# Optimization experiments

Hardware: AMD Instinct MI355X
Metric: run time of the kernel (lower is better)

The kernel has to match this reference:

```python
import jax, jax.numpy as jnp
import numpy as np

VOCAB, EMBED, HIDDEN, LAYERS = 32000, 512, 1024, 2
BATCH, SEQ = 32, 128


def gru_layer(x_tbe, h0, W_ih, W_hh, b_ih, b_hh):
    """x_tbe: [T,B,E_in]; h0: [B,H]. PyTorch GRU gate math."""
    # Precompute input-side gates for all timesteps (one big GEMM).
    gi = jnp.einsum('tbe,ge->tbg', x_tbe, W_ih) + b_ih  # [T,B,3H]

    def step(h, gi_t):
        gh = h @ W_hh.T + b_hh                      # [B,3H]
        i_r, i_z, i_n = jnp.split(gi_t, 3, axis=-1)
        h_r, h_z, h_n = jnp.split(gh, 3, axis=-1)
        r = jax.nn.sigmoid(i_r + h_r)
        z = jax.nn.sigmoid(i_z + h_z)
        n = jnp.tanh(i_n + r * h_n)
        h_new = (1.0 - z) * n + z * h
        return h_new, h_new

    hT, ys = jax.lax.scan(step, h0, gi)
    return ys, hT  # ys: [T,B,H]


def setup_inputs() -> dict:
    key = jax.random.key(0)
    ks = jax.random.split(key, 16)
    s = 0.02
    inp = {
        'inputs': jax.random.randint(ks[0], (BATCH, SEQ), 0, VOCAB),
        'lengths': jax.random.randint(ks[1], (BATCH,), 1, SEQ),
        'hidden': jax.random.normal(ks[2], (LAYERS, BATCH, HIDDEN), jnp.float32),
        'embed_table': jax.random.normal(ks[3], (VOCAB, EMBED), jnp.float32) * s,
        'W_ih_l0': jax.random.normal(ks[4], (3 * HIDDEN, EMBED), jnp.float32) * s,
        'W_hh_l0': jax.random.normal(ks[5], (3 * HIDDEN, HIDDEN), jnp.float32) * s,
        'b_ih_l0': jnp.zeros((3 * HIDDEN,), jnp.float32),
        'b_hh_l0': jnp.zeros((3 * HIDDEN,), jnp.float32),
        'W_ih_l1': jax.random.normal(ks[6], (3 * HIDDEN, HIDDEN), jnp.float32) * s,
        'W_hh_l1': jax.random.normal(ks[7], (3 * HIDDEN, HIDDEN), jnp.float32) * s,
        'b_ih_l1': jnp.zeros((3 * HIDDEN,), jnp.float32),
        'b_hh_l1': jnp.zeros((3 * HIDDEN,), jnp.float32),
        'W_out': jax.random.normal(ks[8], (VOCAB, HIDDEN), jnp.float32) * s,
        'b_out': jnp.zeros((VOCAB,), jnp.float32),
    }
    return inp


def reference(inputs, lengths, hidden, embed_table,
              W_ih_l0, W_hh_l0, b_ih_l0, b_hh_l0,
              W_ih_l1, W_hh_l1, b_ih_l1, b_hh_l1,
              W_out, b_out):
    # embedding: [B,S,E] -> time-major [S,B,E]
    x = embed_table[inputs].transpose(1, 0, 2)
    x, _ = gru_layer(x, hidden[0], W_ih_l0, W_hh_l0, b_ih_l0, b_hh_l0)
    x, _ = gru_layer(x, hidden[1], W_ih_l1, W_hh_l1, b_ih_l1, b_hh_l1)
    outputs = x.transpose(1, 0, 2)                   # [B,S,H]
    logits = outputs @ W_out.T + b_out               # [B,S,V]
    return logits
```

## Files before the change

### kernel.cpp

```cpp
#include <hip/hip_runtime.h>
#include <hip/hip_bf16.h>
#include <stdint.h>

#define T_SEQ 128
#define NBATCH 32
#define EMBED 512
#define HID 1024
#define NVOCAB 32000
#define NBLK 256

typedef float f32x4 __attribute__((ext_vector_type(4)));
typedef _Float16 f16x8 __attribute__((ext_vector_type(8)));

__device__ __forceinline__ unsigned short f2h(float f) {
  _Float16 h = (_Float16)f;
  return __builtin_bit_cast(unsigned short, h);
}
__device__ __forceinline__ float sigm(float x) {
  return 1.0f / (1.0f + __expf(-x));
}
__device__ __forceinline__ float tanh_fast(float x) {
  return 2.0f / (1.0f + __expf(-2.0f * x)) - 1.0f;
}

__global__ void k_zero(unsigned int* __restrict__ p, int n) {
  int i = blockIdx.x * blockDim.x + threadIdx.x;
  if (i < n) p[i] = 0;
}

__global__ void k_f32_to_f16(const float4* __restrict__ in,
                             ushort4* __restrict__ out, int n4) {
  int i = blockIdx.x * blockDim.x + threadIdx.x;
  int stride = gridDim.x * blockDim.x;
  for (; i < n4; i += stride) {
    float4 v = in[i];
    ushort4 o;
    o.x = f2h(v.x); o.y = f2h(v.y); o.z = f2h(v.z); o.w = f2h(v.w);
    out[i] = o;
  }
}

__global__ void k_embed(const int* __restrict__ tok, const float* __restrict__ table,
                        ushort4* __restrict__ A0) {
  int tid = blockIdx.x * 256 + threadIdx.x;
  int m = tid >> 7, kq = tid & 127;
  int b = m & 31, t = m >> 5;
  int tk = tok[b * T_SEQ + t];
  float4 v = *(const float4*)(table + (size_t)tk * EMBED + kq * 4);
  ushort4 o;
  o.x = f2h(v.x); o.y = f2h(v.y); o.z = f2h(v.z); o.w = f2h(v.w);
  A0[tid] = o;
}

#define BM 128
#define BN 128
#define BKK 64

__global__ __launch_bounds__(256) void k_gemm_bt(
    const short* __restrict__ A,
    const short* __restrict__ B,
    float* __restrict__ C,
    const float* __restrict__ bias,
    int M, int N, int K, int permute)
{
  __shared__ __align__(16) short As[BM * BKK];
  __shared__ __align__(16) short Bs[BN * BKK];
  const int tid = threadIdx.x;
  const int w = tid >> 6, l = tid & 63;
  const int wr = w >> 1, wc = w & 1;
  const int bm = blockIdx.x * BM, bn = blockIdx.y * BN;
  const int l15 = l & 15, lkg = l >> 4;

  f32x4 acc[4][4] = {};

  for (int kt = 0; kt < K; kt += BKK) {
#pragma unroll
    for (int p = 0; p < 4; ++p) {
      int idx = p * 2048 + tid * 8;
      int r = idx >> 6, c = idx & 63;
      *(f16x8*)&As[idx] = *(const f16x8*)&A[(size_t)(bm + r) * K + kt + c];
      *(f16x8*)&Bs[idx] = *(const f16x8*)&B[(size_t)(bn + r) * K + kt + c];
    }
    __syncthreads();

#pragma unroll
    for (int ks = 0; ks < 2; ++ks) {
      f16x8 af[4], bfr[4];
#pragma unroll
      for (int mi = 0; mi < 4; ++mi)
        af[mi] = *(const f16x8*)&As[(wr * 64 + mi * 16 + l15) * BKK + ks * 32 + lkg * 8];
#pragma unroll
      for (int ni = 0; ni < 4; ++ni)
        bfr[ni] = *(const f16x8*)&Bs[(wc * 64 + ni * 16 + l15) * BKK + ks * 32 + lkg * 8];
#pragma unroll
      for (int mi = 0; mi < 4; ++mi)
#pragma unroll
        for (int ni = 0; ni < 4; ++ni)
          acc[mi][ni] = __builtin_amdgcn_mfma_f32_16x16x32_f16(
              af[mi], bfr[ni], acc[mi][ni], 0, 0, 0);
    }
    __syncthreads();
  }

  const int lr = lkg * 4;
#pragma unroll
  for (int mi = 0; mi < 4; ++mi) {
#pragma unroll
    for (int ni = 0; ni < 4; ++ni) {
      int col = bn + wc * 64 + ni * 16 + l15;
      float bv = bias ? bias[col] : 0.0f;
#pragma unroll
      for (int j = 0; j < 4; ++j) {
        int row = bm + wr * 64 + mi * 16 + lr + j;
        int orow = permute ? ((row & 31) * T_SEQ + (row >> 5)) : row;
        C[(size_t)orow * N + col] = acc[mi][ni][j] + bv;
      }
    }
  }
}

__global__ __launch_bounds__(384, 2) void k_gru_fused(
    const float* __restrict__ gi0,
    const float* __restrict__ Whh0,
    const float* __restrict__ bhh0,
    const float* __restrict__ Wih1,
    const float* __restrict__ bih1,
    const float* __restrict__ Whh1,
    const float* __restrict__ bhh1,
    const _Float16* __restrict__ h0i,
    const _Float16* __restrict__ h1i,
    _Float16* __restrict__ ys0f,
    _Float16* __restrict__ ys1f,
    unsigned int* flg0,
    unsigned int* flg1,
    unsigned int* epoch0,
    unsigned int* epoch1)
{
  __shared__ float bufIH[2][3][2][64];

  const int tid = threadIdx.x;
  const int l = tid & 63;
  const int w = tid >> 6;
  const int bid = blockIdx.x;
  const int role = w >> 1, nt = w & 1;
  const int j0 = bid * 4;

  const int row16 = l & 15;
  const int jjr = row16 >> 2, gate = row16 & 3;
  const int koct = l >> 4;

  const int b_out = nt * 16 + (l & 15);
  const int j_out = j0 + (l >> 4);
  const int jj_even = (((l >> 4) & 1) == 0);

  const float* Wsrc = (role == 0) ? Whh0 : ((role == 1) ? Wih1 : Whh1);
  f16x8 af[32];
  if (gate < 3) {
    const float* wrow = Wsrc + (size_t)(gate * HID + j0 + jjr) * HID;
#pragma unroll
    for (int c = 0; c < 32; ++c) {
      float4 p0 = *(const float4*)(wrow + c * 32 + koct * 8);
      float4 p1 = *(const float4*)(wrow + c * 32 + koct * 8 + 4);
      f16x8 v = { (_Float16)p0.x, (_Float16)p0.y, (_Float16)p0.z, (_Float16)p0.w,
                  (_Float16)p1.x, (_Float16)p1.y, (_Float16)p1.z, (_Float16)p1.w };
      af[c] = v;
    }
  } else {
#pragma unroll
    for (int c = 0; c < 32; ++c) {
      f16x8 z = { (_Float16)0.f, (_Float16)0.f, (_Float16)0.f, (_Float16)0.f,
                  (_Float16)0.f, (_Float16)0.f, (_Float16)0.f, (_Float16)0.f };
      af[c] = z;
    }
  }

  float bR = 0.f, bZ = 0.f, bN = 0.f, biR = 0.f, biZ = 0.f, biN = 0.f;
  if (role == 0) {
    bR = bhh0[j_out]; bZ = bhh0[HID + j_out]; bN = bhh0[2 * HID + j_out];
  } else if (role == 2) {
    bR = bhh1[j_out]; bZ = bhh1[HID + j_out]; bN = bhh1[2 * HID + j_out];
    biR = bih1[j_out]; biZ = bih1[HID + j_out]; biN = bih1[2 * HID + j_out];
  }

  const int bfragOff = b_out * 2048 + koct * 16;

  const unsigned* ep0 = epoch0 + (bid & 7) * 64;
  const unsigned* ep1 = epoch1 + (bid & 7) * 64;

  for (int s = 0; s <= T_SEQ + 1; ++s) {
    float pre_ir = 0.f, pre_iz = 0.f, pre_in = 0.f;
    if (role == 0 && s < T_SEQ) {
      const float* gib = gi0 + (size_t)(s * NBATCH + b_out) * 3072 + j_out;
      pre_ir = gib[0]; pre_iz = gib[HID]; pre_in = gib[2 * HID];
    }

    if (bid == 0) {
      if (w == 0) {
        unsigned need0 = (s >= 1 && s <= T_SEQ) ? (unsigned)s : 0u;
        unsigned need1 = (s >= 3) ? (unsigned)(s - 2) : 0u;
        if ((need0 | need1) != 0u) {
          const unsigned* f0 = flg0 + l * 8;
          const unsigned* f1 = flg1 + l * 8;
          for (;;) {
            unsigned m0 = 0xffffffffu, m1 = 0xffffffffu;
            if (need0) {
#pragma unroll
              for (int i = 0; i < 8; ++i) {
                unsigned v = __hip_atomic_load(f0 + i, __ATOMIC_RELAXED, __HIP_MEMORY_SCOPE_AGENT);
                m0 = v < m0 ? v : m0;
              }
            }
            if (need1) {
#pragma unroll
              for (int i = 0; i < 8; ++i) {
                unsigned v = __hip_atomic_load(f1 + i, __ATOMIC_RELAXED, __HIP_MEMORY_SCOPE_AGENT);
                m1 = v < m1 ? v : m1;
              }
            }
            if (__all(m0 >= need0 && m1 >= need1)) break;
            __builtin_amdgcn_s_sleep(1);
          }
          if (l < 8) {
            if (need0)
              __hip_atomic_store(epoch0 + l * 64, need0, __ATOMIC_RELAXED, __HIP_MEMORY_SCOPE_AGENT);
            if (need1)
              __hip_atomic_store(epoch1 + l * 64, need1, __ATOMIC_RELAXED, __HIP_MEMORY_SCOPE_AGENT);
          }
          asm volatile("" ::: "memory");
        }
      }
    } else {
      unsigned need = 0;
      const unsigned* ep = ep0;
      if (role == 0) { if (s >= 1 && s < T_SEQ)  need = (unsigned)s; }
      else if (role == 1) { if (s >= 1 && s <= T_SEQ) need = (unsigned)s; }
      else { if (s >= 3) { need = (unsigned)(s - 2); ep = ep1; } }
      if (need) {
        for (;;) {
          unsigned e = __hip_atomic_load(ep, __ATOMIC_RELAXED, __HIP_MEMORY_SCOPE_AGENT);
          if (e >= need) break;
          __builtin_amdgcn_s_sleep(1);
        }
        asm volatile("" ::: "memory");
      }
    }
    __syncthreads();

    if (role == 0 && s < T_SEQ) {
      const _Float16* hsrc = (s == 0) ? h0i : (ys0f + (size_t)(s - 1) * NBATCH * HID);
      const char* hb = (const char*)hsrc + bfragOff;
      f32x4 acc0 = {}, acc1 = {};
#pragma unroll
      for (int c = 0; c < 32; c += 2) {
        f16x8 bf0 = *(const f16x8*)(hb + c * 64);
        f16x8 bf1 = *(const f16x8*)(hb + c * 64 + 64);
        acc0 = __builtin_amdgcn_mfma_f32_16x16x32_f16(af[c], bf0, acc0, 0, 0, 0);
        acc1 = __builtin_amdgcn_mfma_f32_16x16x32_f16(af[c + 1], bf1, acc1, 0, 0, 0);
      }
      f32x4 acc = acc0 + acc1;

      float hp = (float)((s == 0) ? h0i[b_out * HID + j_out]
                                  : ys0f[(size_t)((s - 1) * NBATCH + b_out) * HID + j_out]);
      float r = sigm(pre_ir + acc[0] + bR);
      float z = sigm(pre_iz + acc[1] + bZ);
      float n = tanh_fast(pre_in + r * (acc[2] + bN));
      float hnew = (1.0f - z) * n + z * hp;

      unsigned bits = (unsigned)f2h(hnew);
      unsigned hi = __shfl_down(bits, 16);
      if (jj_even) {
        unsigned packed = (bits & 0xffffu) | (hi << 16);
        __hip_atomic_store((unsigned*)(ys0f + (size_t)(s * NBATCH + b_out) * HID + j_out),
                           packed, __ATOMIC_RELAXED, __HIP_MEMORY_SCOPE_AGENT);
      }
      asm volatile("s_waitcnt vmcnt(0)" ::: "memory");
      if (l == 0)
        __hip_atomic_store(&flg0[bid * 2 + nt], (unsigned)(s + 1),
                           __ATOMIC_RELAXED, __HIP_MEMORY_SCOPE_AGENT);
    }

    if (role == 1 && s >= 1 && s <= T_SEQ) {
      const _Float16* hsrc = ys0f + (size_t)(s - 1) * NBATCH * HID;
      const char* hb = (const char*)hsrc + bfragOff;
      f32x4 acc0 = {}, acc1 = {};
#pragma unroll
      for (int c = 0; c < 32; c += 2) {
        f16x8 bf0 = *(const f16x8*)(hb + c * 64);
        f16x8 bf1 = *(const f16x8*)(hb + c * 64 + 64);
        acc0 = __builtin_amdgcn_mfma_f32_16x16x32_f16(af[c], bf0, acc0, 0, 0, 0);
        acc1 = __builtin_amdgcn_mfma_f32_16x16x32_f16(af[c + 1], bf1, acc1, 0, 0, 0);
      }
      f32x4 acc = acc0 + acc1;
      bufIH[s & 1][0][nt][l] = acc[0];
      bufIH[s & 1][1][nt][l] = acc[1];
      bufIH[s & 1][2][nt][l] = acc[2];
    }

    if (role == 2 && s >= 2) {
      const int t1 = s - 2;
      const _Float16* hsrc = (t1 == 0) ? h1i : (ys1f + (size_t)(t1 - 1) * NBATCH * HID);
      const char* hb = (const char*)hsrc + bfragOff;
      f32x4 acc0 = {}, acc1 = {};
#pragma unroll
      for (int c = 0; c < 32; c += 2) {
        f16x8 bf0 = *(const f16x8*)(hb + c * 64);
        f16x8 bf1 = *(const f16x8*)(hb + c * 64 + 64);
        acc0 = __builtin_amdgcn_mfma_f32_16x16x32_f16(af[c], bf0, acc0, 0, 0, 0);
        acc1 = __builtin_amdgcn_mfma_f32_16x16x32_f16(af[c + 1], bf1, acc1, 0, 0, 0);
      }
      f32x4 acc = acc0 + acc1;

      const int par = (s - 1) & 1;
      float ihR = bufIH[par][0][nt][l] + biR;
      float ihZ = bufIH[par][1][nt][l] + biZ;
      float ihN = bufIH[par][2][nt][l] + biN;
      float hp = (float)((t1 == 0) ? h1i[b_out * HID + j_out]
                                   : ys1f[(size_t)((t1 - 1) * NBATCH + b_out) * HID + j_out]);
      float r = sigm(ihR + acc[0] + bR);
      float z = sigm(ihZ + acc[1] + bZ);
      float n = tanh_fast(ihN + r * (acc[2] + bN));
      float hnew = (1.0f - z) * n + z * hp;

      unsigned bits = (unsigned)f2h(hnew);
      unsigned hi = __shfl_down(bits, 16);
      if (jj_even) {
        unsigned packed = (bits & 0xffffu) | (hi << 16);
        __hip_atomic_store((unsigned*)(ys1f + (size_t)(t1 * NBATCH + b_out) * HID + j_out),
                           packed, __ATOMIC_RELAXED, __HIP_MEMORY_SCOPE_AGENT);
      }
      asm volatile("s_waitcnt vmcnt(0)" ::: "memory");
      if (l == 0)
        __hip_atomic_store(&flg1[bid * 2 + nt], (unsigned)(s - 1),
                           __ATOMIC_RELAXED, __HIP_MEMORY_SCOPE_AGENT);
    }
  }
}

extern "C" void kernel_launch(void* const* d_in, const int* in_sizes, int n_in,
                              void* d_out, int out_size, void* d_ws, size_t ws_size,
                              hipStream_t stream)
{
  const int*   inputs = (const int*)d_in[0];
  const float* hidden = (const float*)d_in[2];
  const float* table  = (const float*)d_in[3];
  const float* Wih0   = (const float*)d_in[4];
  const float* Whh0   = (const float*)d_in[5];
  const float* bih0   = (const float*)d_in[6];
  const float* bhh0   = (const float*)d_in[7];
  const float* Wih1   = (const float*)d_in[8];
  const float* Whh1   = (const float*)d_in[9];
  const float* bih1   = (const float*)d_in[10];
  const float* bhh1   = (const float*)d_in[11];
  const float* Wout   = (const float*)d_in[12];
  const float* bout   = (const float*)d_in[13];
  float* out = (float*)d_out;

  char* ws = (char*)d_ws;
  size_t off = 0;
  auto alloc = [&](size_t bytes) {
    void* p = ws + off;
    off += (bytes + 255) & ~(size_t)255;
    return p;
  };
  float*     gi0  = (float*)alloc((size_t)4096 * 3072 * 4);
  _Float16*  ys0f = (_Float16*)alloc((size_t)4096 * 1024 * 2);
  _Float16*  ys1f = (_Float16*)alloc((size_t)4096 * 1024 * 2);
  short*     A0   = (short*)alloc((size_t)4096 * 512 * 2);
  short*     B0   = (short*)alloc((size_t)3072 * 512 * 2);
  short*     B2   = (short*)alloc((size_t)32000 * 1024 * 2);
  _Float16*  hcat = (_Float16*)alloc((size_t)2 * 32 * 1024 * 2);
  _Float16*  h0i  = hcat;
  _Float16*  h1i  = hcat + 32 * 1024;
  unsigned int* flg0   = (unsigned int*)alloc(512 * 4);
  unsigned int* flg1   = (unsigned int*)alloc(512 * 4);
  unsigned int* epoch0 = (unsigned int*)alloc(512 * 4);
  unsigned int* epoch1 = (unsigned int*)alloc(512 * 4);

  k_zero<<<8, 256, 0, stream>>>(flg0, 2048);

  k_f32_to_f16<<<1024, 256, 0, stream>>>((const float4*)Wih0, (ushort4*)B0, 3072 * 512 / 4);
  k_f32_to_f16<<<2048, 256, 0, stream>>>((const float4*)Wout, (ushort4*)B2, 32000 * 1024 / 4);
  k_f32_to_f16<<<64, 256, 0, stream>>>((const float4*)hidden, (ushort4*)hcat, 2 * 32 * 1024 / 4);
  k_embed<<<2048, 256, 0, stream>>>(inputs, table, (ushort4*)A0);

  dim3 g0(32, 24);
  k_gemm_bt<<<g0, 256, 0, stream>>>(A0, B0, gi0, bih0, 4096, 3072, 512, 0);

  {
    void* kargs[] = {
      (void*)&gi0, (void*)&Whh0, (void*)&bhh0,
      (void*)&Wih1, (void*)&bih1, (void*)&Whh1, (void*)&bhh1,
      (void*)&h0i, (void*)&h1i, (void*)&ys0f, (void*)&ys1f,
      (void*)&flg0, (void*)&flg1, (void*)&epoch0, (void*)&epoch1
    };
    hipError_t e = hipLaunchCooperativeKernel((const void*)k_gru_fused, dim3(NBLK),
                                              dim3(384), kargs, 0, stream);
    if (e != hipSuccess) {
      (void)hipGetLastError();
      k_gru_fused<<<dim3(NBLK), dim3(384), 0, stream>>>(
          gi0, Whh0, bhh0, Wih1, bih1, Whh1, bhh1,
          h0i, h1i, ys0f, ys1f, flg0, flg1, epoch0, epoch1);
    }
  }

  dim3 g2(32, 250);
  k_gemm_bt<<<g2, 256, 0, stream>>>((const short*)ys1f, B2, out, bout, 4096, 32000, 1024, 1);
}
```

Before: 1.802 ms.

## Pad sync flags, spread epoch copies, use direct global-to-LDS loads in GEMM

Pads the per-block progress flags and epoch words to 64-byte strides so each sits on its own cache line. Publishes the epoch to 64 copies instead of 8, which cuts contention among polling blocks. Each waiting block now polls both epochs from a single wave. The GEMM tile loads switch to global_load_lds so data goes straight into LDS without passing through registers. The aim is to lower inter-block barrier latency in the persistent GRU kernel and register pressure in the GEMM, at the cost of more coordinator stores and a changed polling condition.

```diff
diff --git a/kernel.cpp b/kernel.cpp
--- a/kernel.cpp
+++ b/kernel.cpp
@@ -21,6 +21,12 @@
 }
 __device__ __forceinline__ float tanh_fast(float x) {
   return 2.0f / (1.0f + __expf(-2.0f * x)) - 1.0f;
+}
+
+__device__ __forceinline__ void gload_lds16(const void* g, void* l) {
+  __builtin_amdgcn_global_load_lds(
+      (const __attribute__((address_space(1))) void*)g,
+      (__attribute__((address_space(3))) void*)l, 16, 0, 0);
 }
 
 __global__ void k_zero(unsigned int* __restrict__ p, int n) {
@@ -78,8 +84,8 @@
     for (int p = 0; p < 4; ++p) {
       int idx = p * 2048 + tid * 8;
       int r = idx >> 6, c = idx & 63;
-      *(f16x8*)&As[idx] = *(const f16x8*)&A[(size_t)(bm + r) * K + kt + c];
-      *(f16x8*)&Bs[idx] = *(const f16x8*)&B[(size_t)(bn + r) * K + kt + c];
+      gload_lds16(&A[(size_t)(bm + r) * K + kt + c], &As[p * 2048 + w * 512]);
+      gload_lds16(&B[(size_t)(bn + r) * K + kt + c], &Bs[p * 2048 + w * 512]);
     }
     __syncthreads();
 
@@ -184,8 +190,8 @@
 
   const int bfragOff = b_out * 2048 + koct * 16;
 
-  const unsigned* ep0 = epoch0 + (bid & 7) * 64;
-  const unsigned* ep1 = epoch1 + (bid & 7) * 64;
+  const unsigned* ep0 = epoch0 + (bid & 63) * 16;
+  const unsigned* ep1 = epoch1 + (bid & 63) * 16;
 
   for (int s = 0; s <= T_SEQ + 1; ++s) {
     float pre_ir = 0.f, pre_iz = 0.f, pre_in = 0.f;
@@ -194,51 +200,46 @@
       pre_ir = gib[0]; pre_iz = gib[HID]; pre_in = gib[2 * HID];
     }
 
+    unsigned need0 = (s >= 1 && s <= T_SEQ) ? (unsigned)s : 0u;
+    unsigned need1 = (s >= 3) ? (unsigned)(s - 2) : 0u;
+
     if (bid == 0) {
-      if (w == 0) {
-        unsigned need0 = (s >= 1 && s <= T_SEQ) ? (unsigned)s : 0u;
-        unsigned need1 = (s >= 3) ? (unsigned)(s - 2) : 0u;
-        if ((need0 | need1) != 0u) {
-          const unsigned* f0 = flg0 + l * 8;
-          const unsigned* f1 = flg1 + l * 8;
-          for (;;) {
-            unsigned m0 = 0xffffffffu, m1 = 0xffffffffu;
-            if (need0) {
-#pragma unroll
-              for (int i = 0; i < 8; ++i) {
-                unsigned v = __hip_atomic_load(f0 + i, __ATOMIC_RELAXED, __HIP_MEMORY_SCOPE_AGENT);
-                m0 = v < m0 ? v : m0;
-              }
+      if (w == 0 && (need0 | need1) != 0u) {
+        const unsigned* f0 = flg0 + l * 128;
+        const unsigned* f1 = flg1 + l * 128;
+        for (;;) {
+          unsigned m0 = 0xffffffffu, m1 = 0xffffffffu;
+          if (need0) {
+#pragma unroll
+            for (int i = 0; i < 8; ++i) {
+              unsigned v = __hip_atomic_load(f0 + i * 16, __ATOMIC_RELAXED, __HIP_MEMORY_SCOPE_AGENT);
+              m0 = v < m0 ? v : m0;
             }
-            if (need1) {
-#pragma unroll
-              for (int i = 0; i < 8; ++i) {
-                unsigned v = __hip_atomic_load(f1 + i, __ATOMIC_RELAXED, __HIP_MEMORY_SCOPE_AGENT);
-                m1 = v < m1 ? v : m1;
-              }
+          }
+          if (need1) {
+#pragma unroll
+            for (int i = 0; i < 8; ++i) {
+              unsigned v = __hip_atomic_load(f1 + i * 16, __ATOMIC_RELAXED, __HIP_MEMORY_SCOPE_AGENT);
+              m1 = v < m1 ? v : m1;
             }
-            if (__all(m0 >= need0 && m1 >= need1)) break;
-            __builtin_amdgcn_s_sleep(1);
           }
-          if (l < 8) {
-            if (need0)
-              __hip_atomic_store(epoch0 + l * 64, need0, __ATOMIC_RELAXED, __HIP_MEMORY_SCOPE_AGENT);
-            if (need1)
-              __hip_atomic_store(epoch1 + l * 64, need1, __ATOMIC_RELAXED, __HIP_MEMORY_SCOPE_AGENT);
-          }
-          asm volatile("" ::: "memory");
+          if (__all(m0 >= need0 && m1 >= need1)) break;
+          __builtin_amdgcn_s_sleep(1);
         }
+        if (need0)
+          __hip_atomic_store(epoch0 + l * 16, need0, __ATOMIC_RELAXED, __HIP_MEMORY_SCOPE_AGENT);
+        if (need1)
+          __hip_atomic_store(epoch1 + l * 16, need1, __ATOMIC_RELAXED, __HIP_MEMORY_SCOPE_AGENT);
+        asm volatile("" ::: "memory");
       }
     } else {
-      unsigned need = 0;
-      const unsigned* ep = ep0;
-      if (role == 0) { if (s >= 1 && s < T_SEQ)  need = (unsigned)s; }
-      else if (role == 1) { if (s >= 1 && s <= T_SEQ) need = (unsigned)s; }
-      else { if (s >= 3) { need = (unsigned)(s - 2); ep = ep1; } }
-      if (need) {
+      if (w == 0 && (need0 | need1) != 0u) {
         for (;;) {
-          unsigned e = __hip_atomic_load(ep, __ATOMIC_RELAXED, __HIP_MEMORY_SCOPE_AGENT);
-          if (e >= need) break;
+          unsigned a = need0 ? __hip_atomic_load(ep0, __ATOMIC_RELAXED, __HIP_MEMORY_SCOPE_AGENT)
+                             : 0xffffffffu;
+          unsigned b2 = need1 ? __hip_atomic_load(ep1, __ATOMIC_RELAXED, __HIP_MEMORY_SCOPE_AGENT)
+                              : 0xffffffffu;
+          if (a >= need0 && b2 >= need1) break;
           __builtin_amdgcn_s_sleep(1);
         }
         asm volatile("" ::: "memory");
@@ -275,7 +276,7 @@
       }
       asm volatile("s_waitcnt vmcnt(0)" ::: "memory");
       if (l == 0)
-        __hip_atomic_store(&flg0[bid * 2 + nt], (unsigned)(s + 1),
+        __hip_atomic_store(&flg0[(bid * 2 + nt) * 16], (unsigned)(s + 1),
                            __ATOMIC_RELAXED, __HIP_MEMORY_SCOPE_AGENT);
     }
 
@@ -330,7 +331,7 @@
       }
       asm volatile("s_waitcnt vmcnt(0)" ::: "memory");
       if (l == 0)
-        __hip_atomic_store(&flg1[bid * 2 + nt], (unsigned)(s - 1),
+        __hip_atomic_store(&flg1[(bid * 2 + nt) * 16], (unsigned)(s - 1),
                            __ATOMIC_RELAXED, __HIP_MEMORY_SCOPE_AGENT);
     }
   }
@@ -371,12 +372,12 @@
   _Float16*  hcat = (_Float16*)alloc((size_t)2 * 32 * 1024 * 2);
   _Float16*  h0i  = hcat;
   _Float16*  h1i  = hcat + 32 * 1024;
-  unsigned int* flg0   = (unsigned int*)alloc(512 * 4);
-  unsigned int* flg1   = (unsigned int*)alloc(512 * 4);
-  unsigned int* epoch0 = (unsigned int*)alloc(512 * 4);
-  unsigned int* epoch1 = (unsigned int*)alloc(512 * 4);
-
-  k_zero<<<8, 256, 0, stream>>>(flg0, 2048);
+  unsigned int* flg0   = (unsigned int*)alloc(512 * 16 * 4);
+  unsigned int* flg1   = (unsigned int*)alloc(512 * 16 * 4);
+  unsigned int* epoch0 = (unsigned int*)alloc(64 * 16 * 4);
+  unsigned int* epoch1 = (unsigned int*)alloc(64 * 16 * 4);
+
+  k_zero<<<72, 256, 0, stream>>>(flg0, 18432);
 
   k_f32_to_f16<<<1024, 256, 0, stream>>>((const float4*)Wih0, (ushort4*)B0, 3072 * 512 / 4);
   k_f32_to_f16<<<2048, 256, 0, stream>>>((const float4*)Wout, (ushort4*)B2, 32000 * 1024 / 4);
```

Result: slower. 1.912 ms (+6.1%).
